# Optimization experiments

Hardware: AMD Instinct MI355X
Metric: run time of the kernel (lower is better)

The kernel has to match this reference:

```python
import jax, jax.numpy as jnp
import numpy as np

INPUT_DIM = 512
HIDDEN_DIM = 1024
OUTPUT_DIM = 512
SEQ_LEN = 16384


def setup_inputs() -> dict:
    key = jax.random.key(0)
    ks = jax.random.split(key, 8)
    s = 1.0 / np.sqrt(HIDDEN_DIM)
    X = jax.random.normal(ks[0], (SEQ_LEN, INPUT_DIM), dtype=jnp.float32)
    # PyTorch GRU params: weight_ih [3H, D], weight_hh [3H, H], biases [3H]; gate order r, z, n
    W_ih = jax.random.uniform(ks[1], (3 * HIDDEN_DIM, INPUT_DIM), minval=-s, maxval=s, dtype=jnp.float32)
    W_hh = jax.random.uniform(ks[2], (3 * HIDDEN_DIM, HIDDEN_DIM), minval=-s, maxval=s, dtype=jnp.float32)
    b_ih = jax.random.uniform(ks[3], (3 * HIDDEN_DIM,), minval=-s, maxval=s, dtype=jnp.float32)
    b_hh = jax.random.uniform(ks[4], (3 * HIDDEN_DIM,), minval=-s, maxval=s, dtype=jnp.float32)
    W_fc = jax.random.uniform(ks[5], (OUTPUT_DIM, HIDDEN_DIM), minval=-s, maxval=s, dtype=jnp.float32)
    b_fc = jax.random.uniform(ks[6], (OUTPUT_DIM,), minval=-s, maxval=s, dtype=jnp.float32)
    return {"X": X, "W_ih": W_ih, "W_hh": W_hh, "b_ih": b_ih, "b_hh": b_hh, "W_fc": W_fc, "b_fc": b_fc}


def _gru_seq(X, W_ih, W_hh, b_ih, b_hh):
    H = W_hh.shape[1]
    # Precompute input projections for all timesteps in one GEMM: [T, 3H]
    gx = X @ W_ih.T + b_ih

    def step(h, gx_t):
        gxr, gxz, gxn = gx_t[:H], gx_t[H:2 * H], gx_t[2 * H:]
        gh = h @ W_hh.T + b_hh
        ghr, ghz, ghn = gh[:H], gh[H:2 * H], gh[2 * H:]
        r = jax.nn.sigmoid(gxr + ghr)
        z = jax.nn.sigmoid(gxz + ghz)
        n = jnp.tanh(gxn + r * ghn)
        h_new = (1.0 - z) * n + z * h
        return h_new, h_new

    h0 = jnp.zeros((H,), dtype=X.dtype)
    _, hs = jax.lax.scan(step, h0, gx)  # hs: [T, H]
    return hs


def reference(X, W_ih, W_hh, b_ih, b_hh, W_fc, b_fc):
    hs = _gru_seq(X, W_ih, W_hh, b_ih, b_hh)  # [T, H]
    return hs @ W_fc.T + b_fc  # [T, output_dim]
```

## Files before the change

### kernel.cpp

```cpp
#include <hip/hip_runtime.h>
#include <hip/hip_bf16.h>

#define H      1024
#define IN_DIM 512
#define OD     512
#define T_LEN  16384
#define NWG    256
#define NREP   16
#define RS     (H + 64)
#define PSTRIDE (NREP * RS)

typedef unsigned long long u64;
typedef unsigned int u32;

__device__ __forceinline__ u32 pack_bf(float lo, float hi) {
    u32 a = __float_as_uint(lo); a = (a + 0x7fffu + ((a >> 16) & 1u)) >> 16;
    u32 b = __float_as_uint(hi); b = (b + 0x7fffu + ((b >> 16) & 1u)) & 0xffff0000u;
    return a | b;
}
__device__ __forceinline__ float bf_lo(u32 pk) { return __uint_as_float(pk << 16); }
__device__ __forceinline__ float bf_hi(u32 pk) { return __uint_as_float(pk & 0xffff0000u); }

__global__ __launch_bounds__(256, 1)
void gru_rec_kernel(const float* __restrict__ X,
                    const float* __restrict__ Wih,
                    const float* __restrict__ Whh,
                    const float* __restrict__ bih,
                    const float* __restrict__ bhh,
                    float* __restrict__ hs,
                    u32* __restrict__ vals)
{
    const int tid  = threadIdx.x;
    const int wave = tid >> 6;
    const int lane = tid & 63;
    const int wg   = blockIdx.x;
    const int gw   = wg * 4 + wave;
    const int u    = gw;

    u32 whh_r[3][8];
    u32 wih_r[3][4];
    #pragma unroll
    for (int g = 0; g < 3; ++g) {
        const float* wr = Whh + (size_t)(g * H + u) * H;
        #pragma unroll
        for (int k = 0; k < 8; ++k)
            whh_r[g][k] = pack_bf(wr[2 * lane + 128 * k], wr[2 * lane + 1 + 128 * k]);
        const float* wx = Wih + (size_t)(g * H + u) * IN_DIM;
        #pragma unroll
        for (int k = 0; k < 4; ++k)
            wih_r[g][k] = pack_bf(wx[2 * lane + 128 * k], wx[2 * lane + 1 + 128 * k]);
    }
    const float bxr = bih[u], bxz = bih[H + u], bxn = bih[2 * H + u];
    const float bhr = bhh[u], bhz = bhh[H + u], bhn = bhh[2 * H + u];

    float xv[8], xw[8];
    #pragma unroll
    for (int k = 0; k < 4; ++k) {
        float2 v = *(const float2*)(X + 2 * lane + 128 * k);
        xv[2 * k] = v.x; xv[2 * k + 1] = v.y;
    }

    const int rep = gw & (NREP - 1);
    float hmine = 0.f;

    #pragma unroll 1
    for (int t = 0; t < T_LEN; ++t) {
        float xr = 0.f, xz = 0.f, xn = 0.f;
        #pragma unroll
        for (int k = 0; k < 4; ++k) {
            const float x0 = xv[2 * k], x1 = xv[2 * k + 1];
            xr += bf_lo(wih_r[0][k]) * x0 + bf_hi(wih_r[0][k]) * x1;
            xz += bf_lo(wih_r[1][k]) * x0 + bf_hi(wih_r[1][k]) * x1;
            xn += bf_lo(wih_r[2][k]) * x0 + bf_hi(wih_r[2][k]) * x1;
        }
        float xns = xn;
        #pragma unroll
        for (int s = 32; s; s >>= 1) xns += __shfl_xor(xns, s, 64);

        {
            const int tn = (t + 1 < T_LEN) ? (t + 1) : t;
            const float* xp = X + (size_t)tn * IN_DIM;
            #pragma unroll
            for (int k = 0; k < 4; ++k) {
                float2 v = *(const float2*)(xp + 2 * lane + 128 * k);
                xw[2 * k] = v.x; xw[2 * k + 1] = v.y;
            }
        }

        const u32 lapexp = (u32)((t >> 1) & 1);
        const u64* pb = (const u64*)(vals + (size_t)(t & 1) * PSTRIDE
                                          + (size_t)rep * RS) + lane;
        u64 v[8];
        for (;;) {
            #pragma unroll
            for (int k = 0; k < 8; ++k)
                v[k] = __hip_atomic_load(pb + 64 * k, __ATOMIC_RELAXED,
                                         __HIP_MEMORY_SCOPE_AGENT);
            u32 bad = 0;
            #pragma unroll
            for (int k = 0; k < 8; ++k)
                bad |= ((u32)v[k] ^ lapexp) | ((u32)(v[k] >> 32) ^ lapexp);
            if (!(bad & 1u)) break;
        }

        if (t && gw == ((t - 1) & (H - 1))) {
            u64* dst = (u64*)(hs + (size_t)(t - 1) * H) + lane;
            #pragma unroll
            for (int k = 0; k < 8; ++k) dst[64 * k] = v[k];
        }

        float ar = xr, az = xz, anh = 0.f;
        #pragma unroll
        for (int k = 0; k < 8; ++k) {
            const float h0 = __uint_as_float((u32)v[k]);
            const float h1 = __uint_as_float((u32)(v[k] >> 32));
            ar  += bf_lo(whh_r[0][k]) * h0 + bf_hi(whh_r[0][k]) * h1;
            az  += bf_lo(whh_r[1][k]) * h0 + bf_hi(whh_r[1][k]) * h1;
            anh += bf_lo(whh_r[2][k]) * h0 + bf_hi(whh_r[2][k]) * h1;
        }
        #pragma unroll
        for (int s = 32; s; s >>= 1) {
            ar  += __shfl_xor(ar,  s, 64);
            az  += __shfl_xor(az,  s, 64);
            anh += __shfl_xor(anh, s, 64);
        }

        const float r = 1.f / (1.f + __expf(-(ar + bxr + bhr)));
        const float z = 1.f / (1.f + __expf(-(az + bxz + bhz)));
        const float e2 = __expf(2.f * (xns + bxn + r * (anh + bhn)));
        const float n = 1.f - 2.f / (e2 + 1.f);
        const float hnew = (1.f - z) * n + z * hmine;
        const u32 lapw = (u32)(((t + 1) >> 1) & 1);
        const u32 bits = (__float_as_uint(hnew) & ~1u) | lapw;
        hmine = __uint_as_float(bits);
        if (lane < NREP)
            __hip_atomic_store(vals + (size_t)((t + 1) & 1) * PSTRIDE
                                    + (size_t)lane * RS + u,
                               bits, __ATOMIC_RELAXED, __HIP_MEMORY_SCOPE_AGENT);
        if (t == T_LEN - 1 && lane == 0)
            hs[(size_t)t * H + u] = hmine;

        #pragma unroll
        for (int i = 0; i < 8; ++i) xv[i] = xw[i];
    }
}

#define BM 64
#define BN 64
#define BK 16
__global__ __launch_bounds__(256)
void fc_kernel(const float* __restrict__ A, const float* __restrict__ B,
               const float* __restrict__ bias, float* __restrict__ C)
{
    __shared__ float As[BK][BM + 4];
    __shared__ float Bs[BK][BN + 4];
    const int tid = threadIdx.x;
    const int m0 = blockIdx.y * BM, n0 = blockIdx.x * BN;
    const int tx = tid & 15, ty = tid >> 4;
    float acc[4][4] = {};
    const int r = tid >> 2, c = (tid & 3) << 2;
    for (int k0 = 0; k0 < H; k0 += BK) {
        float4 va = *(const float4*)(A + (size_t)(m0 + r) * H + (k0 + c));
        As[c + 0][r] = va.x; As[c + 1][r] = va.y; As[c + 2][r] = va.z; As[c + 3][r] = va.w;
        float4 vb = *(const float4*)(B + (size_t)(n0 + r) * H + (k0 + c));
        Bs[c + 0][r] = vb.x; Bs[c + 1][r] = vb.y; Bs[c + 2][r] = vb.z; Bs[c + 3][r] = vb.w;
        __syncthreads();
        #pragma unroll
        for (int kk = 0; kk < BK; ++kk) {
            float4 a4 = *(const float4*)&As[kk][ty * 4];
            float4 b4 = *(const float4*)&Bs[kk][tx * 4];
            const float av[4] = {a4.x, a4.y, a4.z, a4.w};
            const float bv[4] = {b4.x, b4.y, b4.z, b4.w};
            #pragma unroll
            for (int i = 0; i < 4; ++i)
                #pragma unroll
                for (int j = 0; j < 4; ++j)
                    acc[i][j] += av[i] * bv[j];
        }
        __syncthreads();
    }
    #pragma unroll
    for (int i = 0; i < 4; ++i) {
        const int m = m0 + ty * 4 + i;
        #pragma unroll
        for (int j = 0; j < 4; ++j) {
            const int n = n0 + tx * 4 + j;
            C[(size_t)m * OD + n] = acc[i][j] + bias[n];
        }
    }
}

extern "C" void kernel_launch(void* const* d_in, const int* in_sizes, int n_in,
                              void* d_out, int out_size, void* d_ws, size_t ws_size,
                              hipStream_t stream) {
    const float* X   = (const float*)d_in[0];
    const float* Wih = (const float*)d_in[1];
    const float* Whh = (const float*)d_in[2];
    const float* bih = (const float*)d_in[3];
    const float* bhh = (const float*)d_in[4];
    const float* Wfc = (const float*)d_in[5];
    const float* bfc = (const float*)d_in[6];
    float* out = (float*)d_out;

    float* hs  = (float*)d_ws;
    u32*  vals = (u32*)((char*)d_ws + (size_t)T_LEN * H * 4);

    hipMemsetAsync(vals, 0x00, (size_t)PSTRIDE * 4, stream);
    hipMemsetAsync(vals + PSTRIDE, 0x01, (size_t)PSTRIDE * 4, stream);

    void* args[] = { (void*)&X, (void*)&Wih, (void*)&Whh, (void*)&bih,
                     (void*)&bhh, (void*)&hs, (void*)&vals };
    hipError_t e = hipLaunchCooperativeKernel((const void*)gru_rec_kernel,
                                              dim3(NWG), dim3(256), args, 0, stream);
    if (e != hipSuccess) {
        gru_rec_kernel<<<dim3(NWG), dim3(256), 0, stream>>>(X, Wih, Whh, bih, bhh, hs, vals);
    }

    dim3 fgrid(OD / BN, T_LEN / BM);
    fc_kernel<<<fgrid, dim3(256), 0, stream>>>(hs, Wfc, bfc, out);
}
```

Measured before the change: 28.60 ms.

## Poll global h-state with one wave per workgroup and broadcast via LDS

Only wave 0 of each workgroup now spins on the global replicated hidden-state buffer. It forwards the values through a double-buffered LDS array, and the other three waves spin on that LDS copy instead of on global memory. This cuts global/L2 polling traffic by a factor of four and is meant to reduce contention on the per-step barrier. The input projection for step t+1 is also moved after the h-update, so it runs off the critical path between the store and the next poll. The cost is an added LDS hop on the critical path, and correctness now depends on workgroup-scope atomics and the lap-bit encoding in LDS.

```diff
diff --git a/kernel.cpp b/kernel.cpp
--- a/kernel.cpp
+++ b/kernel.cpp
@@ -30,6 +30,8 @@
                     float* __restrict__ hs,
                     u32* __restrict__ vals)
 {
+    __shared__ u64 lsh[2][8][64];
+
     const int tid  = threadIdx.x;
     const int wave = tid >> 6;
     const int lane = tid & 63;
@@ -53,63 +55,91 @@
     const float bxr = bih[u], bxz = bih[H + u], bxn = bih[2 * H + u];
     const float bhr = bhh[u], bhz = bhh[H + u], bhn = bhh[2 * H + u];
 
-    float xv[8], xw[8];
+    {
+        u32* lp = (u32*)lsh;
+        for (int i = tid; i < 2048; i += 256) lp[i] = (i < 1024) ? 0u : 1u;
+    }
+    __syncthreads();
+
+    float xw[8];
     #pragma unroll
     for (int k = 0; k < 4; ++k) {
-        float2 v = *(const float2*)(X + 2 * lane + 128 * k);
-        xv[2 * k] = v.x; xv[2 * k + 1] = v.y;
-    }
-
-    const int rep = gw & (NREP - 1);
+        float2 vv = *(const float2*)(X + 2 * lane + 128 * k);
+        xw[2 * k] = vv.x; xw[2 * k + 1] = vv.y;
+    }
+    float pxr = 0.f, pxz = 0.f, pxns = 0.f;
+    {
+        float xn = 0.f;
+        #pragma unroll
+        for (int k = 0; k < 4; ++k) {
+            const float x0 = xw[2 * k], x1 = xw[2 * k + 1];
+            pxr += bf_lo(wih_r[0][k]) * x0 + bf_hi(wih_r[0][k]) * x1;
+            pxz += bf_lo(wih_r[1][k]) * x0 + bf_hi(wih_r[1][k]) * x1;
+            xn  += bf_lo(wih_r[2][k]) * x0 + bf_hi(wih_r[2][k]) * x1;
+        }
+        #pragma unroll
+        for (int s = 32; s; s >>= 1) xn += __shfl_xor(xn, s, 64);
+        pxns = xn;
+    }
+
+    const int rep = wg & (NREP - 1);
     float hmine = 0.f;
 
     #pragma unroll 1
     for (int t = 0; t < T_LEN; ++t) {
-        float xr = 0.f, xz = 0.f, xn = 0.f;
-        #pragma unroll
-        for (int k = 0; k < 4; ++k) {
-            const float x0 = xv[2 * k], x1 = xv[2 * k + 1];
-            xr += bf_lo(wih_r[0][k]) * x0 + bf_hi(wih_r[0][k]) * x1;
-            xz += bf_lo(wih_r[1][k]) * x0 + bf_hi(wih_r[1][k]) * x1;
-            xn += bf_lo(wih_r[2][k]) * x0 + bf_hi(wih_r[2][k]) * x1;
-        }
-        float xns = xn;
-        #pragma unroll
-        for (int s = 32; s; s >>= 1) xns += __shfl_xor(xns, s, 64);
-
+        const u32 lapexp = (u32)((t >> 1) & 1);
+        const int p = t & 1;
+        u64 v[8];
+
+        if (wave == 0) {
+            const u64* pb = (const u64*)(vals + (size_t)p * PSTRIDE
+                                              + (size_t)rep * RS) + lane;
+            for (;;) {
+                #pragma unroll
+                for (int k = 0; k < 8; ++k)
+                    v[k] = __hip_atomic_load(pb + 64 * k, __ATOMIC_RELAXED,
+                                             __HIP_MEMORY_SCOPE_AGENT);
+                u32 bad = 0;
+                #pragma unroll
+                for (int k = 0; k < 8; ++k)
+                    bad |= ((u32)v[k] ^ lapexp) | ((u32)(v[k] >> 32) ^ lapexp);
+                if (!(bad & 1u)) break;
+            }
+            #pragma unroll
+            for (int k = 0; k < 8; ++k)
+                __hip_atomic_store(&lsh[p][k][lane], v[k], __ATOMIC_RELAXED,
+                                   __HIP_MEMORY_SCOPE_WORKGROUP);
+        } else {
+            for (;;) {
+                u32 bad = 0;
+                #pragma unroll
+                for (int k = 0; k < 8; ++k) {
+                    v[k] = __hip_atomic_load(&lsh[p][k][lane], __ATOMIC_RELAXED,
+                                             __HIP_MEMORY_SCOPE_WORKGROUP);
+                    bad |= ((u32)v[k] ^ lapexp) | ((u32)(v[k] >> 32) ^ lapexp);
+                }
+                if (!(bad & 1u)) break;
+            }
+        }
+
+        if (t && wave == 1 && wg == ((t - 1) & 255)) {
+            u64* dst = (u64*)(hs + (size_t)(t - 1) * H) + lane;
+            #pragma unroll
+            for (int k = 0; k < 8; ++k) dst[64 * k] = v[k];
+        }
+
+        float xn2[8];
         {
             const int tn = (t + 1 < T_LEN) ? (t + 1) : t;
             const float* xp = X + (size_t)tn * IN_DIM;
             #pragma unroll
             for (int k = 0; k < 4; ++k) {
-                float2 v = *(const float2*)(xp + 2 * lane + 128 * k);
-                xw[2 * k] = v.x; xw[2 * k + 1] = v.y;
-            }
-        }
-
-        const u32 lapexp = (u32)((t >> 1) & 1);
-        const u64* pb = (const u64*)(vals + (size_t)(t & 1) * PSTRIDE
-                                          + (size_t)rep * RS) + lane;
-        u64 v[8];
-        for (;;) {
-            #pragma unroll
-            for (int k = 0; k < 8; ++k)
-                v[k] = __hip_atomic_load(pb + 64 * k, __ATOMIC_RELAXED,
-                                         __HIP_MEMORY_SCOPE_AGENT);
-            u32 bad = 0;
-            #pragma unroll
-            for (int k = 0; k < 8; ++k)
-                bad |= ((u32)v[k] ^ lapexp) | ((u32)(v[k] >> 32) ^ lapexp);
-            if (!(bad & 1u)) break;
-        }
-
-        if (t && gw == ((t - 1) & (H - 1))) {
-            u64* dst = (u64*)(hs + (size_t)(t - 1) * H) + lane;
-            #pragma unroll
-            for (int k = 0; k < 8; ++k) dst[64 * k] = v[k];
-        }
-
-        float ar = xr, az = xz, anh = 0.f;
+                float2 vv = *(const float2*)(xp + 2 * lane + 128 * k);
+                xn2[2 * k] = vv.x; xn2[2 * k + 1] = vv.y;
+            }
+        }
+
+        float ar = pxr, az = pxz, anh = 0.f;
         #pragma unroll
         for (int k = 0; k < 8; ++k) {
             const float h0 = __uint_as_float((u32)v[k]);
@@ -127,7 +157,7 @@
 
         const float r = 1.f / (1.f + __expf(-(ar + bxr + bhr)));
         const float z = 1.f / (1.f + __expf(-(az + bxz + bhz)));
-        const float e2 = __expf(2.f * (xns + bxn + r * (anh + bhn)));
+        const float e2 = __expf(2.f * (pxns + bxn + r * (anh + bhn)));
         const float n = 1.f - 2.f / (e2 + 1.f);
         const float hnew = (1.f - z) * n + z * hmine;
         const u32 lapw = (u32)(((t + 1) >> 1) & 1);
@@ -140,8 +170,19 @@
         if (t == T_LEN - 1 && lane == 0)
             hs[(size_t)t * H + u] = hmine;
 
-        #pragma unroll
-        for (int i = 0; i < 8; ++i) xv[i] = xw[i];
+        {
+            float xr2 = 0.f, xz2 = 0.f, xn3 = 0.f;
+            #pragma unroll
+            for (int k = 0; k < 4; ++k) {
+                const float x0 = xn2[2 * k], x1 = xn2[2 * k + 1];
+                xr2 += bf_lo(wih_r[0][k]) * x0 + bf_hi(wih_r[0][k]) * x1;
+                xz2 += bf_lo(wih_r[1][k]) * x0 + bf_hi(wih_r[1][k]) * x1;
+                xn3 += bf_lo(wih_r[2][k]) * x0 + bf_hi(wih_r[2][k]) * x1;
+            }
+            #pragma unroll
+            for (int s = 32; s; s >>= 1) xn3 += __shfl_xor(xn3, s, 64);
+            pxr = xr2; pxz = xz2; pxns = xn3;
+        }
     }
 }
 
```

Result: no change. 28.74 ms (+0.5%).
